# Kernel tuning notes

Hardware: AMD Instinct MI355X
Metric: run time of the kernel (lower is better)

## Reference

```python
import jax, jax.numpy as jnp
import numpy as np

B, C, H, W, Q = 4, 64, 128, 128, 65536
HID, OUT = 256, 3
IN_DIM = C + 4  # q_feat (C) + rel coord (2) + cell (2)


def setup_inputs() -> dict:
    key = jax.random.key(0)
    ks = jax.random.split(key, 16)
    feat = jax.random.normal(ks[0], (B, C, H, W), dtype=jnp.float32)
    s_grid = jax.random.uniform(ks[1], (B, Q, 2), dtype=jnp.float32, minval=-1.0, maxval=1.0)
    # cell size of a 256x256 output image in [-1,1] coords: 2/256 per axis
    s_cell = jnp.full((B, Q, 2), 2.0 / 256.0, dtype=jnp.float32)
    dims = [IN_DIM, HID, HID, HID, HID, OUT]
    inp = {"feat": feat, "s_grid": s_grid, "s_cell": s_cell}
    for i in range(5):
        inp[f"w{i}"] = 0.02 * jax.random.normal(ks[2 + 2 * i], (dims[i], dims[i + 1]), dtype=jnp.float32)
        inp[f"b{i}"] = jnp.zeros((dims[i + 1],), dtype=jnp.float32)
    return inp


def reference(feat, s_grid, s_cell, w0, b0, w1, b1, w2, b2, w3, b3, w4, b4):
    Bf, Cf, Hf, Wf = feat.shape
    eps = 1e-6
    dh, dw = 1.0 / Hf, 1.0 / Wf
    dt = feat.dtype
    # q_cell scaled by feature resolution
    qc = s_cell * jnp.asarray([Hf, Wf], dtype=dt)  # [B,Q,2]
    feat_flat = feat.reshape(Bf, Cf, Hf * Wf)
    ws, bs = [w0, w1, w2, w3], [b0, b1, b2, b3]

    preds, areas = [], []
    for r in (-1.0, 1.0):
        for c in (-1.0, 1.0):
            # shifted, clamped query grid (channel 0 = h/y, channel 1 = w/x)
            gy = jnp.clip(s_grid[..., 0] + r * dh, -1.0 + eps, 1.0 - eps)
            gx = jnp.clip(s_grid[..., 1] + c * dw, -1.0 + eps, 1.0 - eps)
            # grid_sample nearest, align_corners=False: unnormalize then round (half-even, as nearbyint)
            iy = jnp.clip(jnp.round(((gy + 1.0) * Hf - 1.0) * 0.5).astype(jnp.int32), 0, Hf - 1)
            ix = jnp.clip(jnp.round(((gx + 1.0) * Wf - 1.0) * 0.5).astype(jnp.int32), 0, Wf - 1)
            lin = iy * Wf + ix  # [B,Q]
            q_feat = jnp.take_along_axis(feat_flat, lin[:, None, :], axis=2).transpose(0, 2, 1)  # [B,Q,C]
            # coord of the gathered pixel center (= grid_sample of make_coord feat_grid)
            py = -1.0 + (2.0 * iy.astype(dt) + 1.0) / Hf
            px = -1.0 + (2.0 * ix.astype(dt) + 1.0) / Wf
            rel_y = (s_grid[..., 0] - py) * Hf
            rel_x = (s_grid[..., 1] - px) * Wf
            rel = jnp.stack([rel_y, rel_x], axis=-1)  # [B,Q,2]
            h = jnp.concatenate([q_feat, rel, qc], axis=-1)  # [B,Q,C+4]
            for wl, bl in zip(ws, bs):
                h = jax.nn.relu(h @ wl + bl)
            pred = h @ w4 + b4  # [B,Q,OUT]
            preds.append(pred)
            areas.append(jnp.abs(rel_y * rel_x) + 1e-9)

    total = areas[0] + areas[1] + areas[2] + areas[3]
    # LIIF swaps diagonally-opposite areas: 0<->3, 1<->2
    areas = [areas[3], areas[2], areas[1], areas[0]]
    ret = preds[0] * (areas[0] / total)[..., None]
    for p, a in zip(preds[1:], areas[1:]):
        ret = ret + p * (a / total)[..., None]
    return ret
```

## Files before the change

kernel.cpp:

```cpp
#include <hip/hip_runtime.h>


typedef _Float16 half8 __attribute__((ext_vector_type(8)));
typedef float f32x4 __attribute__((ext_vector_type(4)));

#define ROWS     256
#define THREADS  1024

#define A_BYTES    131072
#define AREA_OFF   131072
#define PRED_OFF   132096
#define SMEM_BYTES 136192

static __device__ __forceinline__ unsigned short f2h(float f) {
    union { _Float16 h; unsigned short u; } v;
    v.h = (_Float16)f;
    return v.u;
}

#define SWZ(row, byte) ((byte) ^ (((row) & 7) << 4))

static __device__ __host__ __forceinline__ int PI(int p) {
    return ((p >> 6) << 6) | ((p & 15) << 2) | ((p >> 4) & 3);
}

__global__ void transpose_feat(const float* __restrict__ feat,
                               unsigned short* __restrict__ featT) {
    __shared__ float tile[64][65];
    const int bi  = blockIdx.x;
    const int b   = bi >> 8;
    const int rem = bi & 255;
    const int y   = rem >> 1;
    const int xc  = (rem & 1) << 6;
    const int tid = threadIdx.x;

    {
        const int x  = tid & 63;
        const int cg = tid >> 6;
#pragma unroll
        for (int i = 0; i < 16; ++i) {
            int c = cg * 16 + i;
            tile[c][x] = feat[(((b << 6) + c) << 14) + (y << 7) + xc + x];
        }
    }
    __syncthreads();
    {
        const int c  = tid & 63;
        const int xg = tid >> 6;
#pragma unroll
        for (int i = 0; i < 16; ++i) {
            int xx = xg * 16 + i;
            featT[(size_t)((((b << 7) + y) << 7) + xc + xx) * 64 + c] =
                f2h(tile[c][xx]);
        }
    }
}

__global__ void pack_w(const float* __restrict__ src,
                       unsigned short* __restrict__ dst,
                       int K, int N, int ksteps, int nct, int permN) {
    int tid = blockIdx.x * 256 + threadIdx.x;
    int total = ksteps * nct * 512;
    if (tid >= total) return;
    int j    = tid & 7;
    int lane = (tid >> 3) & 63;
    int f    = tid >> 9;
    int ct   = f % nct;
    int ks   = f / nct;
    int k = ks * 32 + ((lane >> 4) << 3) + j;
    int n = ct * 16 + (lane & 15);
    int ns = permN ? PI(n) : n;
    float v = (k < K && ns < N) ? src[k * N + ns] : 0.0f;
    dst[tid] = f2h(v);
}

template <int NP>
static __device__ __forceinline__ void layer_step(
    char* A, const unsigned short* __restrict__ wsel,
    const float* __restrict__ bsel,
    int lane, int wm, int wn) {

    const int l15 = lane & 15;
    f32x4 acc[4][4];
#pragma unroll
    for (int rf = 0; rf < 4; ++rf)
#pragma unroll
        for (int cf = 0; cf < 4; ++cf)
            acc[rf][cf] = (f32x4){0.f, 0.f, 0.f, 0.f};

#pragma unroll 2
    for (int kp = 0; kp < NP; ++kp) {
        half8 af[4];
        const int kbyte = (kp << 6) + ((lane >> 4) << 4);
        const int xorv  = (lane & 7) << 4;
#pragma unroll
        for (int rf = 0; rf < 4; ++rf) {
            int row = wm * 64 + rf * 16 + l15;
            af[rf] = *(const half8*)(A + row * 512 + (kbyte ^ xorv));
        }
#pragma unroll
        for (int cf = 0; cf < 4; ++cf) {
            half8 bf = *(const half8*)(wsel + (size_t)((kp * 16 + wn * 4 + cf) * 64 + lane) * 8);
#pragma unroll
            for (int rf = 0; rf < 4; ++rf)
                acc[rf][cf] = __builtin_amdgcn_mfma_f32_16x16x32_f16(
                    af[rf], bf, acc[rf][cf], 0, 0, 0);
        }
    }
    __syncthreads();

    const float4 bias = *(const float4*)(bsel + wn * 64 + l15 * 4);
    const int colbyte = (wn << 7) + (l15 << 3);

#pragma unroll
    for (int rf = 0; rf < 4; ++rf) {
        const int rbase = wm * 64 + rf * 16 + ((lane >> 4) << 2);
#pragma unroll
        for (int q = 0; q < 4; ++q) {
            const int row = rbase + q;
            union { _Float16 h[4]; uint2 u; } pk;
            pk.h[0] = (_Float16)fmaxf(acc[rf][0][q] + bias.x, 0.0f);
            pk.h[1] = (_Float16)fmaxf(acc[rf][1][q] + bias.y, 0.0f);
            pk.h[2] = (_Float16)fmaxf(acc[rf][2][q] + bias.z, 0.0f);
            pk.h[3] = (_Float16)fmaxf(acc[rf][3][q] + bias.w, 0.0f);
            *(uint2*)(A + row * 512 + (colbyte ^ ((row & 7) << 4))) = pk.u;
        }
    }
    __syncthreads();
}

__global__ __launch_bounds__(1024, 4) void mlp_main(
    const unsigned short* __restrict__ featT,
    const float* __restrict__ sgrid,
    const float* __restrict__ scell,
    const unsigned short* __restrict__ wp0, const unsigned short* __restrict__ wp1,
    const unsigned short* __restrict__ wp2, const unsigned short* __restrict__ wp3,
    const unsigned short* __restrict__ wp4,
    const float* __restrict__ bp0, const float* __restrict__ bp1,
    const float* __restrict__ bp2, const float* __restrict__ bp3,
    const float* __restrict__ bp4,
    float* __restrict__ out) {

    extern __shared__ char lds[];
    char*  A     = lds;
    float* areas = (float*)(lds + AREA_OFF);
    float* predl = (float*)(lds + PRED_OFF);

    const int tid  = threadIdx.x;
    const int lane = tid & 63;
    const int wv   = tid >> 6;
    const int wm   = wv >> 2;
    const int wn   = wv & 3;

    if (tid < 512) {
        const int row  = tid >> 1;
        const int half = tid & 1;
        const int grow = blockIdx.x * ROWS + row;
        const int qq   = grow >> 2;
        const int s    = grow & 3;
        const int b    = qq >> 16;

        const float g0 = sgrid[qq * 2 + 0];
        const float g1 = sgrid[qq * 2 + 1];
        const float c0 = scell[qq * 2 + 0];
        const float c1 = scell[qq * 2 + 1];

        const float rs = (s & 2) ? 1.0f : -1.0f;
        const float cs = (s & 1) ? 1.0f : -1.0f;
        const float dh = 0.0078125f;
        const float LO = (float)(-1.0 + 1e-6);
        const float HI = (float)( 1.0 - 1e-6);

        float gy = fminf(fmaxf(g0 + rs * dh, LO), HI);
        float gx = fminf(fmaxf(g1 + cs * dh, LO), HI);
        float ty = ((gy + 1.0f) * 128.0f - 1.0f) * 0.5f;
        float tx = ((gx + 1.0f) * 128.0f - 1.0f) * 0.5f;
        int iy = (int)rintf(ty); iy = min(max(iy, 0), 127);
        int ix = (int)rintf(tx); ix = min(max(ix, 0), 127);

        float py = -1.0f + (float)(2 * iy + 1) * 0.0078125f;
        float px = -1.0f + (float)(2 * ix + 1) * 0.0078125f;
        float rel_y = (g0 - py) * 128.0f;
        float rel_x = (g1 - px) * 128.0f;
        float qcy = c0 * 128.0f;
        float qcx = c1 * 128.0f;

        if (half == 0) areas[row] = fabsf(rel_y * rel_x) + 1e-9f;

        const unsigned short* src =
            featT + (size_t)((((b << 7) + iy) << 7) + ix) * 64 + (half << 5);
        uint4 v0 = *(const uint4*)(src + 0);
        uint4 v1 = *(const uint4*)(src + 8);
        uint4 v2 = *(const uint4*)(src + 16);
        uint4 v3 = *(const uint4*)(src + 24);

        char* arow = A + row * 512;
        const int kb0 = half << 6;
        *(uint4*)(arow + SWZ(row, kb0 +  0)) = v0;
        *(uint4*)(arow + SWZ(row, kb0 + 16)) = v1;
        *(uint4*)(arow + SWZ(row, kb0 + 32)) = v2;
        *(uint4*)(arow + SWZ(row, kb0 + 48)) = v3;

        if (half) {
            uint4 t;
            t.x = (unsigned)f2h(rel_y) | ((unsigned)f2h(rel_x) << 16);
            t.y = (unsigned)f2h(qcy)   | ((unsigned)f2h(qcx)   << 16);
            t.z = 0; t.w = 0;
            uint4 z = {0, 0, 0, 0};
            *(uint4*)(arow + SWZ(row, 128)) = t;
            *(uint4*)(arow + SWZ(row, 144)) = z;
            *(uint4*)(arow + SWZ(row, 160)) = z;
            *(uint4*)(arow + SWZ(row, 176)) = z;
        }
    }
    __syncthreads();

    layer_step<3>(A, wp0, bp0, lane, wm, wn);
    layer_step<8>(A, wp1, bp1, lane, wm, wn);
    layer_step<8>(A, wp2, bp2, lane, wm, wn);
    layer_step<8>(A, wp3, bp3, lane, wm, wn);

    {
        f32x4 a4 = (f32x4){0.f, 0.f, 0.f, 0.f};
        const int xorv = (lane & 7) << 4;
#pragma unroll
        for (int kp = 0; kp < 8; ++kp) {
            const int kbyte = (kp << 6) + ((lane >> 4) << 4);
            half8 b = *(const half8*)(wp4 + (size_t)((kp * 64) + lane) * 8);
            int row = wv * 16 + (lane & 15);
            half8 a = *(const half8*)(A + row * 512 + (kbyte ^ xorv));
            a4 = __builtin_amdgcn_mfma_f32_16x16x32_f16(a, b, a4, 0, 0, 0);
        }
        __syncthreads();

        const int col = lane & 15;
        const float b4v = (col < 3) ? bp4[col] : 0.0f;
        if (col < 3) {
#pragma unroll
            for (int q = 0; q < 4; ++q) {
                int row = wv * 16 + ((lane >> 4) << 2) + q;
                predl[row * 4 + col] = a4[q] + b4v;
            }
        }
        __syncthreads();

        if (tid < 192) {
            int qloc = tid / 3;
            int c    = tid - qloc * 3;
            int r0   = qloc * 4;
            float a0 = areas[r0 + 0], a1 = areas[r0 + 1];
            float a2 = areas[r0 + 2], a3 = areas[r0 + 3];
            float total = ((a0 + a1) + a2) + a3;
            float ret = predl[(r0 + 0) * 4 + c] * (a3 / total);
            ret      += predl[(r0 + 1) * 4 + c] * (a2 / total);
            ret      += predl[(r0 + 2) * 4 + c] * (a1 / total);
            ret      += predl[(r0 + 3) * 4 + c] * (a0 / total);
            int qq0 = blockIdx.x * 64 + qloc;
            out[qq0 * 3 + c] = ret;
        }
    }
}

extern "C" void kernel_launch(void* const* d_in, const int* in_sizes, int n_in,
                              void* d_out, int out_size, void* d_ws, size_t ws_size,
                              hipStream_t stream) {
    const float* feat  = (const float*)d_in[0];
    const float* sgrid = (const float*)d_in[1];
    const float* scell = (const float*)d_in[2];
    const float* w0 = (const float*)d_in[3];
    const float* b0 = (const float*)d_in[4];
    const float* w1 = (const float*)d_in[5];
    const float* b1 = (const float*)d_in[6];
    const float* w2 = (const float*)d_in[7];
    const float* b2 = (const float*)d_in[8];
    const float* w3 = (const float*)d_in[9];
    const float* b3 = (const float*)d_in[10];
    const float* w4 = (const float*)d_in[11];
    const float* b4 = (const float*)d_in[12];

    char* ws = (char*)d_ws;
    unsigned short* featT = (unsigned short*)ws;
    unsigned short* wp0 = (unsigned short*)(ws + 8388608);
    unsigned short* wp1 = (unsigned short*)(ws + 8388608 + 49152);
    unsigned short* wp2 = (unsigned short*)(ws + 8388608 + 49152 + 131072);
    unsigned short* wp3 = (unsigned short*)(ws + 8388608 + 49152 + 2 * 131072);
    unsigned short* wp4 = (unsigned short*)(ws + 8388608 + 49152 + 3 * 131072);

    transpose_feat<<<1024, 256, 0, stream>>>(feat, featT);
    pack_w<<<96,  256, 0, stream>>>(w0, wp0,  68, 256, 3, 16, 1);
    pack_w<<<256, 256, 0, stream>>>(w1, wp1, 256, 256, 8, 16, 1);
    pack_w<<<256, 256, 0, stream>>>(w2, wp2, 256, 256, 8, 16, 1);
    pack_w<<<256, 256, 0, stream>>>(w3, wp3, 256, 256, 8, 16, 1);
    pack_w<<<16,  256, 0, stream>>>(w4, wp4, 256, 3, 8, 1, 0);

    hipFuncSetAttribute(reinterpret_cast<const void*>(mlp_main),
                        hipFuncAttributeMaxDynamicSharedMemorySize, SMEM_BYTES);
    mlp_main<<<4096, THREADS, SMEM_BYTES, stream>>>(
        featT, sgrid, scell, wp0, wp1, wp2, wp3, wp4,
        b0, b1, b2, b3, b4, (float*)d_out);
}
```

Before: 463.6 us.

## Replace block-wide barriers with per-row-group LDS atomic flag barriers

Swaps the two __syncthreads per MLP layer for counters in LDS, one pair per 64-row group of four waves, so each row group waits only on the waves that share its rows. It also drops the barrier after the final-layer MFMA. The goal is to let different row groups run out of step and cut stalls from block-wide barriers. In exchange it adds atomic traffic and spin-waits with s_sleep. Dropping the last barrier may be a race, because wave wv reads rows wv*16.. that other waves in the group just wrote, and predl overlaps nothing. It is probably safe, since the wflag wait covers the reads.

```diff
diff --git a/kernel.cpp b/kernel.cpp
--- a/kernel.cpp
+++ b/kernel.cpp
@@ -10,7 +10,8 @@
 #define A_BYTES    131072
 #define AREA_OFF   131072
 #define PRED_OFF   132096
-#define SMEM_BYTES 136192
+#define FLAG_OFF   136192
+#define SMEM_BYTES 136224
 
 static __device__ __forceinline__ unsigned short f2h(float f) {
     union { _Float16 h; unsigned short u; } v;
@@ -76,7 +77,8 @@
 
 template <int NP>
 static __device__ __forceinline__ void layer_step(
-    char* A, const unsigned short* __restrict__ wsel,
+    char* A, int* rflag, int* wflag, int target,
+    const unsigned short* __restrict__ wsel,
     const float* __restrict__ bsel,
     int lane, int wm, int wn) {
 
@@ -107,7 +109,13 @@
                     af[rf], bf, acc[rf][cf], 0, 0, 0);
         }
     }
-    __syncthreads();
+
+    if (lane == 0)
+        __hip_atomic_fetch_add(rflag, 1, __ATOMIC_RELEASE,
+                               __HIP_MEMORY_SCOPE_WORKGROUP);
+    while (__hip_atomic_load(rflag, __ATOMIC_ACQUIRE,
+                             __HIP_MEMORY_SCOPE_WORKGROUP) < target)
+        __builtin_amdgcn_s_sleep(1);
 
     const float4 bias = *(const float4*)(bsel + wn * 64 + l15 * 4);
     const int colbyte = (wn << 7) + (l15 << 3);
@@ -126,7 +134,13 @@
             *(uint2*)(A + row * 512 + (colbyte ^ ((row & 7) << 4))) = pk.u;
         }
     }
-    __syncthreads();
+
+    if (lane == 0)
+        __hip_atomic_fetch_add(wflag, 1, __ATOMIC_RELEASE,
+                               __HIP_MEMORY_SCOPE_WORKGROUP);
+    while (__hip_atomic_load(wflag, __ATOMIC_ACQUIRE,
+                             __HIP_MEMORY_SCOPE_WORKGROUP) < target)
+        __builtin_amdgcn_s_sleep(1);
 }
 
 __global__ __launch_bounds__(1024, 4) void mlp_main(
@@ -145,12 +159,15 @@
     char*  A     = lds;
     float* areas = (float*)(lds + AREA_OFF);
     float* predl = (float*)(lds + PRED_OFF);
+    int*   flags = (int*)(lds + FLAG_OFF);
 
     const int tid  = threadIdx.x;
     const int lane = tid & 63;
     const int wv   = tid >> 6;
     const int wm   = wv >> 2;
     const int wn   = wv & 3;
+
+    if (tid < 8) flags[tid] = 0;
 
     if (tid < 512) {
         const int row  = tid >> 1;
@@ -215,10 +232,12 @@
     }
     __syncthreads();
 
-    layer_step<3>(A, wp0, bp0, lane, wm, wn);
-    layer_step<8>(A, wp1, bp1, lane, wm, wn);
-    layer_step<8>(A, wp2, bp2, lane, wm, wn);
-    layer_step<8>(A, wp3, bp3, lane, wm, wn);
+    int* rflag = &flags[wm];
+    int* wflag = &flags[4 + wm];
+    layer_step<3>(A, rflag, wflag,  4, wp0, bp0, lane, wm, wn);
+    layer_step<8>(A, rflag, wflag,  8, wp1, bp1, lane, wm, wn);
+    layer_step<8>(A, rflag, wflag, 12, wp2, bp2, lane, wm, wn);
+    layer_step<8>(A, rflag, wflag, 16, wp3, bp3, lane, wm, wn);
 
     {
         f32x4 a4 = (f32x4){0.f, 0.f, 0.f, 0.f};
@@ -231,7 +250,6 @@
             half8 a = *(const half8*)(A + row * 512 + (kbyte ^ xorv));
             a4 = __builtin_amdgcn_mfma_f32_16x16x32_f16(a, b, a4, 0, 0, 0);
         }
-        __syncthreads();
 
         const int col = lane & 15;
         const float b4v = (col < 3) ? bp4[col] : 0.0f;
```

After: 449.5 us. 3.0% less time.
